# Kernel optimization log

Hardware: AMD Instinct MI355X
Metric: run time of the kernel (lower is better)

Reference implementation:

```python
import jax, jax.numpy as jnp
import numpy as np

B = 64        # number of graphs in the batch
NPG = 1024    # nodes per graph (uniform batch_num_nodes)
N = B * NPG   # total nodes = 65536
D = 512       # input feature dim
DEG = 32      # average degree
K = 0.5       # keep-percent
DROP = NPG - int(np.ceil(K * NPG))  # number of lowest-score nodes zeroed per graph


def setup_inputs() -> dict:
    key = jax.random.key(0)
    k1, k2, k3, k4 = jax.random.split(key, 4)
    features = jax.random.normal(k1, (N, D), dtype=jnp.float32)
    # edges constrained inside each graph's node block (batched DGL graph is block-diagonal)
    offsets = (jnp.arange(B, dtype=jnp.int64) * NPG)[:, None]
    src = (jax.random.randint(k2, (B, NPG * DEG), 0, NPG, dtype=jnp.int64) + offsets).reshape(-1)
    dst = (jax.random.randint(k3, (B, NPG * DEG), 0, NPG, dtype=jnp.int64) + offsets).reshape(-1)
    # GraphConv(input_dim=D, out=1) parameters (glorot-ish scale)
    weight = jax.random.normal(k4, (D, 1), dtype=jnp.float32) * (1.0 / np.sqrt(D))
    bias = jnp.zeros((1,), dtype=jnp.float32)
    return {"features": features, "src": src, "dst": dst, "weight": weight, "bias": bias}


def reference(features, src, dst, weight, bias):
    # --- GraphConv(D -> 1, norm=True, bias=True, activation=relu) ---
    # old-DGL norm=True: symmetric normalization with in-degrees, norm=deg^-0.5 (0 for isolated)
    deg = jnp.zeros((N,), features.dtype).at[dst].add(1.0)
    norm = jnp.where(deg > 0, deg ** -0.5, 0.0)[:, None]          # [N,1]
    # in_feats > out_feats: project first, then aggregate scalars
    h = (features @ weight) * norm                                # [N,1]
    agg = jnp.zeros_like(h).at[dst].add(h[src])                   # sum over in-edges
    w = jax.nn.relu(agg * norm + bias)                            # [N,1] scores
    # --- per-graph top-k masking: zero the DROP smallest scores in each graph ---
    wb = w.reshape(B, NPG)
    ranks = jnp.argsort(jnp.argsort(wb, axis=1), axis=1)          # rank 0 = smallest
    wb = jnp.where(ranks < DROP, jnp.zeros((), wb.dtype), wb)
    # --- elementwise gating of features by (masked) scores ---
    return features * wb.reshape(N, 1)
```

## Files before the change

kernel.cpp:

```cpp
#include <hip/hip_runtime.h>

#define NTOT 65536
#define DIM  512
#define BGR  64
#define NPG  1024
#define DROPN 512
#define SLICES 8
#define MV_BLOCKS 2048

typedef float vf4 __attribute__((ext_vector_type(4)));
typedef unsigned long long u64;

__global__ __launch_bounds__(256) void k1_matvec_deg(
        const float* __restrict__ X, const float* __restrict__ W,
        const int* __restrict__ dst,
        float* __restrict__ p, int* __restrict__ deg_part, int epg) {
    __shared__ int dl[NPG];
    if (blockIdx.x < MV_BLOCKS) {
        const int lane = threadIdx.x & 63;
        const int wid  = (blockIdx.x * 256 + threadIdx.x) >> 6;
        const int nw   = (MV_BLOCKS * 256) >> 6;
        const vf4* wr = (const vf4*)W;
        const vf4 w0 = wr[lane], w1 = wr[lane + 64];
        for (int row = wid; row < NTOT; row += 2 * nw) {
            const int row2 = row + nw;
            const vf4* xr0 = (const vf4*)(X + (size_t)row  * DIM);
            const vf4* xr1 = (const vf4*)(X + (size_t)row2 * DIM);
            vf4 a0 = xr0[lane], a1 = xr0[lane + 64];
            vf4 b0 = xr1[lane], b1 = xr1[lane + 64];
            vf4 m0 = a0 * w0 + a1 * w1;
            vf4 m1 = b0 * w0 + b1 * w1;
            float s0 = m0[0] + m0[1] + m0[2] + m0[3];
            float s1 = m1[0] + m1[1] + m1[2] + m1[3];
            #pragma unroll
            for (int off = 32; off > 0; off >>= 1) {
                s0 += __shfl_down(s0, off, 64);
                s1 += __shfl_down(s1, off, 64);
            }
            if (lane == 0) { p[row] = s0; p[row2] = s1; }
        }
    } else {
        const int b = blockIdx.x - MV_BLOCKS;
        const int g = b & (BGR - 1);
        const int slice = b >> 6;
        const int nbase = g * NPG;
        const int eps = epg / SLICES;
        for (int i = threadIdx.x; i < NPG; i += 256) dl[i] = 0;
        __syncthreads();
        const int4* d4 = (const int4*)(dst + (size_t)g * epg + (size_t)slice * eps);
        const int n4 = eps >> 2;
        for (int i = threadIdx.x; i < n4; i += 256) {
            int4 d = d4[i];
            atomicAdd(&dl[d.x - nbase], 1);
            atomicAdd(&dl[d.y - nbase], 1);
            atomicAdd(&dl[d.z - nbase], 1);
            atomicAdd(&dl[d.w - nbase], 1);
        }
        __syncthreads();
        int* out = deg_part + (size_t)slice * NTOT + nbase;
        for (int i = threadIdx.x; i < NPG; i += 256) out[i] = dl[i];
    }
}

__global__ __launch_bounds__(256) void k2_agg(
        const int* __restrict__ src, const int* __restrict__ dst,
        const float* __restrict__ p, const int* __restrict__ deg_part,
        float* __restrict__ agg_part, float* __restrict__ norm_out, int epg) {
    __shared__ float hl[NPG];
    __shared__ float al[NPG];
    const int b = blockIdx.x;
    const int g = b & (BGR - 1);
    const int slice = b >> 6;
    const int nbase = g * NPG;
    const int eps = epg / SLICES;
    for (int i = threadIdx.x; i < NPG; i += 256) {
        int d = 0;
        #pragma unroll
        for (int s = 0; s < SLICES; s++) d += deg_part[(size_t)s * NTOT + nbase + i];
        float nrm = d > 0 ? (1.0f / sqrtf((float)d)) : 0.f;
        hl[i] = p[nbase + i] * nrm;
        al[i] = 0.f;
        if (slice == 0) norm_out[nbase + i] = nrm;
    }
    __syncthreads();
    const int4* s4 = (const int4*)(src + (size_t)g * epg + (size_t)slice * eps);
    const int4* d4 = (const int4*)(dst + (size_t)g * epg + (size_t)slice * eps);
    const int n4 = eps >> 2;
    for (int i = threadIdx.x; i < n4; i += 256) {
        int4 s = s4[i];
        int4 d = d4[i];
        atomicAdd(&al[d.x - nbase], hl[s.x - nbase]);
        atomicAdd(&al[d.y - nbase], hl[s.y - nbase]);
        atomicAdd(&al[d.z - nbase], hl[s.z - nbase]);
        atomicAdd(&al[d.w - nbase], hl[s.w - nbase]);
    }
    __syncthreads();
    float* out = agg_part + (size_t)slice * NTOT + nbase;
    for (int i = threadIdx.x; i < NPG; i += 256) out[i] = al[i];
}

__global__ __launch_bounds__(1024) void k3_topk(
        const float* __restrict__ agg_part, const float* __restrict__ norm,
        const float* __restrict__ bias, float* __restrict__ gate) {
    __shared__ u64 sk[NPG];
    const int g = blockIdx.x;
    const int t = threadIdx.x;
    const int nbase = g * NPG;
    float a = 0.f;
    #pragma unroll
    for (int s = 0; s < SLICES; s++) a += agg_part[(size_t)s * NTOT + nbase + t];
    float w = a * norm[nbase + t] + bias[0];
    w = w > 0.f ? w : 0.f;
    u64 key = ((u64)__float_as_uint(w) << 32) | (unsigned int)t;

    for (int k = 2; k <= NPG; k <<= 1) {
        const bool up = ((t & k) == 0);
        for (int j = k >> 1; j >= 64; j >>= 1) {
            sk[t] = key;
            __syncthreads();
            u64 partner = sk[t ^ j];
            __syncthreads();
            bool takeMin = (((t & j) == 0) == up);
            key = takeMin ? (key < partner ? key : partner)
                          : (key > partner ? key : partner);
        }
        for (int j = ((k >> 1) < 32 ? (k >> 1) : 32); j >= 1; j >>= 1) {
            u64 partner = (u64)__shfl_xor((long long)key, j, 64);
            bool takeMin = (((t & j) == 0) == up);
            key = takeMin ? (key < partner ? key : partner)
                          : (key > partner ? key : partner);
        }
    }
    int idx = (int)(key & 0xffffffffull);
    float wv = __uint_as_float((unsigned int)(key >> 32));
    gate[nbase + idx] = (t < DROPN) ? 0.f : wv;
}

__global__ __launch_bounds__(256) void k4_gate(
        const float* __restrict__ X, const float* __restrict__ gate,
        float* __restrict__ out) {
    const int lane = threadIdx.x & 63;
    const int nw   = (gridDim.x * blockDim.x) >> 6;
    const int wid  = (blockIdx.x * blockDim.x + threadIdx.x) >> 6;
    for (int row = wid; row < NTOT; row += nw) {
        float g = gate[row];
        vf4* o = (vf4*)(out + (size_t)row * DIM);
        if (g == 0.f) {
            vf4 z = (vf4){0.f, 0.f, 0.f, 0.f};
            o[lane] = z;
            o[lane + 64] = z;
        } else {
            const vf4* xr = (const vf4*)(X + (size_t)row * DIM);
            o[lane]      = xr[lane] * g;
            o[lane + 64] = xr[lane + 64] * g;
        }
    }
}

extern "C" void kernel_launch(void* const* d_in, const int* in_sizes, int n_in,
                              void* d_out, int out_size, void* d_ws, size_t ws_size,
                              hipStream_t stream) {
    const float* X    = (const float*)d_in[0];
    const int*   src  = (const int*)d_in[1];
    const int*   dst  = (const int*)d_in[2];
    const float* W    = (const float*)d_in[3];
    const float* bias = (const float*)d_in[4];
    float* out = (float*)d_out;
    int E   = in_sizes[1];
    int epg = E / BGR;

    float* ws       = (float*)d_ws;
    float* p        = ws;
    float* norm     = ws + 1 * NTOT;
    float* gate     = ws + 2 * NTOT;
    int*   deg_part = (int*)(ws + 3 * NTOT);
    float* agg_part = ws + (3 + SLICES) * NTOT;

    k1_matvec_deg<<<MV_BLOCKS + BGR * SLICES, 256, 0, stream>>>(X, W, dst, p, deg_part, epg);
    k2_agg<<<BGR * SLICES, 256, 0, stream>>>(src, dst, p, deg_part, agg_part, norm, epg);
    k3_topk<<<BGR, 1024, 0, stream>>>(agg_part, norm, bias, gate);
    k4_gate<<<2048, 256, 0, stream>>>(X, gate, out);
}
```

Measured before the change: 280.2 us.

## Fuse all four stages into one cooperative kernel with grid syncs

```diff
diff --git a/kernel.cpp b/kernel.cpp
--- a/kernel.cpp
+++ b/kernel.cpp
@@ -1,29 +1,44 @@
 #include <hip/hip_runtime.h>
+#include <hip/hip_cooperative_groups.h>
+
+namespace cg = cooperative_groups;
 
 #define NTOT 65536
 #define DIM  512
 #define BGR  64
 #define NPG  1024
 #define DROPN 512
-#define SLICES 8
-#define MV_BLOCKS 2048
+#define SLICES 4
+#define NBLK 256
+#define NTHR 1024
 
 typedef float vf4 __attribute__((ext_vector_type(4)));
 typedef unsigned long long u64;
 
-__global__ __launch_bounds__(256) void k1_matvec_deg(
+__global__ __launch_bounds__(NTHR, 4) void fused_all(
         const float* __restrict__ X, const float* __restrict__ W,
-        const int* __restrict__ dst,
-        float* __restrict__ p, int* __restrict__ deg_part, int epg) {
-    __shared__ int dl[NPG];
-    if (blockIdx.x < MV_BLOCKS) {
-        const int lane = threadIdx.x & 63;
-        const int wid  = (blockIdx.x * 256 + threadIdx.x) >> 6;
-        const int nw   = (MV_BLOCKS * 256) >> 6;
+        const int* __restrict__ src, const int* __restrict__ dst,
+        const float* __restrict__ bias,
+        float* __restrict__ p, float* __restrict__ norm,
+        int* __restrict__ deg_part, float* __restrict__ agg_part,
+        float* __restrict__ gate, float* __restrict__ out, int epg) {
+    cg::grid_group grid = cg::this_grid();
+    __shared__ u64 smem64[NPG];
+
+    const int t       = threadIdx.x;
+    const int lane    = t & 63;
+    const int gw      = blockIdx.x * (NTHR / 64) + (t >> 6);
+    const int NW      = NBLK * (NTHR / 64);
+    const int g       = blockIdx.x & (BGR - 1);
+    const int slice   = blockIdx.x >> 6;
+    const int nbase   = g * NPG;
+    const int eps     = epg / SLICES;
+
+    {
         const vf4* wr = (const vf4*)W;
         const vf4 w0 = wr[lane], w1 = wr[lane + 64];
-        for (int row = wid; row < NTOT; row += 2 * nw) {
-            const int row2 = row + nw;
+        for (int row = gw; row < NTOT; row += 2 * NW) {
+            const int row2 = row + NW;
             const vf4* xr0 = (const vf4*)(X + (size_t)row  * DIM);
             const vf4* xr1 = (const vf4*)(X + (size_t)row2 * DIM);
             vf4 a0 = xr0[lane], a1 = xr0[lane + 64];
@@ -39,17 +54,15 @@
             }
             if (lane == 0) { p[row] = s0; p[row2] = s1; }
         }
-    } else {
-        const int b = blockIdx.x - MV_BLOCKS;
-        const int g = b & (BGR - 1);
-        const int slice = b >> 6;
-        const int nbase = g * NPG;
-        const int eps = epg / SLICES;
-        for (int i = threadIdx.x; i < NPG; i += 256) dl[i] = 0;
+    }
+
+    {
+        int* dl = (int*)smem64;
+        for (int i = t; i < NPG; i += NTHR) dl[i] = 0;
         __syncthreads();
         const int4* d4 = (const int4*)(dst + (size_t)g * epg + (size_t)slice * eps);
         const int n4 = eps >> 2;
-        for (int i = threadIdx.x; i < n4; i += 256) {
+        for (int i = t; i < n4; i += NTHR) {
             int4 d = d4[i];
             atomicAdd(&dl[d.x - nbase], 1);
             atomicAdd(&dl[d.y - nbase], 1);
@@ -57,102 +70,85 @@
             atomicAdd(&dl[d.w - nbase], 1);
         }
         __syncthreads();
-        int* out = deg_part + (size_t)slice * NTOT + nbase;
-        for (int i = threadIdx.x; i < NPG; i += 256) out[i] = dl[i];
+        int* op = deg_part + (size_t)slice * NTOT + nbase;
+        for (int i = t; i < NPG; i += NTHR) op[i] = dl[i];
     }
-}
+    grid.sync();
 
-__global__ __launch_bounds__(256) void k2_agg(
-        const int* __restrict__ src, const int* __restrict__ dst,
-        const float* __restrict__ p, const int* __restrict__ deg_part,
-        float* __restrict__ agg_part, float* __restrict__ norm_out, int epg) {
-    __shared__ float hl[NPG];
-    __shared__ float al[NPG];
-    const int b = blockIdx.x;
-    const int g = b & (BGR - 1);
-    const int slice = b >> 6;
-    const int nbase = g * NPG;
-    const int eps = epg / SLICES;
-    for (int i = threadIdx.x; i < NPG; i += 256) {
-        int d = 0;
+    {
+        float* hl = (float*)smem64;
+        float* al = ((float*)smem64) + NPG;
+        for (int i = t; i < NPG; i += NTHR) {
+            int d = 0;
+            #pragma unroll
+            for (int s = 0; s < SLICES; s++) d += deg_part[(size_t)s * NTOT + nbase + i];
+            float nr = d > 0 ? (1.0f / sqrtf((float)d)) : 0.f;
+            hl[i] = p[nbase + i] * nr;
+            al[i] = 0.f;
+            if (slice == 0) norm[nbase + i] = nr;
+        }
+        __syncthreads();
+        const int4* s4 = (const int4*)(src + (size_t)g * epg + (size_t)slice * eps);
+        const int4* d4 = (const int4*)(dst + (size_t)g * epg + (size_t)slice * eps);
+        const int n4 = eps >> 2;
+        for (int i = t; i < n4; i += NTHR) {
+            int4 s = s4[i];
+            int4 d = d4[i];
+            atomicAdd(&al[d.x - nbase], hl[s.x - nbase]);
+            atomicAdd(&al[d.y - nbase], hl[s.y - nbase]);
+            atomicAdd(&al[d.z - nbase], hl[s.z - nbase]);
+            atomicAdd(&al[d.w - nbase], hl[s.w - nbase]);
+        }
+        __syncthreads();
+        float* op = agg_part + (size_t)slice * NTOT + nbase;
+        for (int i = t; i < NPG; i += NTHR) op[i] = al[i];
+    }
+    grid.sync();
+
+    if (blockIdx.x < BGR) {
+        u64* sk = smem64;
+        const int nb2 = blockIdx.x * NPG;
+        float a = 0.f;
         #pragma unroll
-        for (int s = 0; s < SLICES; s++) d += deg_part[(size_t)s * NTOT + nbase + i];
-        float nrm = d > 0 ? (1.0f / sqrtf((float)d)) : 0.f;
-        hl[i] = p[nbase + i] * nrm;
-        al[i] = 0.f;
-        if (slice == 0) norm_out[nbase + i] = nrm;
+        for (int s = 0; s < SLICES; s++) a += agg_part[(size_t)s * NTOT + nb2 + t];
+        float w = a * norm[nb2 + t] + bias[0];
+        w = w > 0.f ? w : 0.f;
+        u64 key = ((u64)__float_as_uint(w) << 32) | (unsigned int)t;
+        for (int k = 2; k <= NPG; k <<= 1) {
+            const bool up = ((t & k) == 0);
+            for (int j = k >> 1; j >= 64; j >>= 1) {
+                sk[t] = key;
+                __syncthreads();
+                u64 partner = sk[t ^ j];
+                __syncthreads();
+                bool takeMin = (((t & j) == 0) == up);
+                key = takeMin ? (key < partner ? key : partner)
+                              : (key > partner ? key : partner);
+            }
+            for (int j = ((k >> 1) < 32 ? (k >> 1) : 32); j >= 1; j >>= 1) {
+                u64 partner = (u64)__shfl_xor((long long)key, j, 64);
+                bool takeMin = (((t & j) == 0) == up);
+                key = takeMin ? (key < partner ? key : partner)
+                              : (key > partner ? key : partner);
+            }
+        }
+        int idx = (int)(key & 0xffffffffull);
+        float wv = __uint_as_float((unsigned int)(key >> 32));
+        gate[nb2 + idx] = (t < DROPN) ? 0.f : wv;
     }
-    __syncthreads();
-    const int4* s4 = (const int4*)(src + (size_t)g * epg + (size_t)slice * eps);
-    const int4* d4 = (const int4*)(dst + (size_t)g * epg + (size_t)slice * eps);
-    const int n4 = eps >> 2;
-    for (int i = threadIdx.x; i < n4; i += 256) {
-        int4 s = s4[i];
-        int4 d = d4[i];
-        atomicAdd(&al[d.x - nbase], hl[s.x - nbase]);
-        atomicAdd(&al[d.y - nbase], hl[s.y - nbase]);
-        atomicAdd(&al[d.z - nbase], hl[s.z - nbase]);
-        atomicAdd(&al[d.w - nbase], hl[s.w - nbase]);
-    }
-    __syncthreads();
-    float* out = agg_part + (size_t)slice * NTOT + nbase;
-    for (int i = threadIdx.x; i < NPG; i += 256) out[i] = al[i];
-}
+    grid.sync();
 
-__global__ __launch_bounds__(1024) void k3_topk(
-        const float* __restrict__ agg_part, const float* __restrict__ norm,
-        const float* __restrict__ bias, float* __restrict__ gate) {
-    __shared__ u64 sk[NPG];
-    const int g = blockIdx.x;
-    const int t = threadIdx.x;
-    const int nbase = g * NPG;
-    float a = 0.f;
-    #pragma unroll
-    for (int s = 0; s < SLICES; s++) a += agg_part[(size_t)s * NTOT + nbase + t];
-    float w = a * norm[nbase + t] + bias[0];
-    w = w > 0.f ? w : 0.f;
-    u64 key = ((u64)__float_as_uint(w) << 32) | (unsigned int)t;
-
-    for (int k = 2; k <= NPG; k <<= 1) {
-        const bool up = ((t & k) == 0);
-        for (int j = k >> 1; j >= 64; j >>= 1) {
-            sk[t] = key;
-            __syncthreads();
-            u64 partner = sk[t ^ j];
-            __syncthreads();
-            bool takeMin = (((t & j) == 0) == up);
-            key = takeMin ? (key < partner ? key : partner)
-                          : (key > partner ? key : partner);
-        }
-        for (int j = ((k >> 1) < 32 ? (k >> 1) : 32); j >= 1; j >>= 1) {
-            u64 partner = (u64)__shfl_xor((long long)key, j, 64);
-            bool takeMin = (((t & j) == 0) == up);
-            key = takeMin ? (key < partner ? key : partner)
-                          : (key > partner ? key : partner);
-        }
-    }
-    int idx = (int)(key & 0xffffffffull);
-    float wv = __uint_as_float((unsigned int)(key >> 32));
-    gate[nbase + idx] = (t < DROPN) ? 0.f : wv;
-}
-
-__global__ __launch_bounds__(256) void k4_gate(
-        const float* __restrict__ X, const float* __restrict__ gate,
-        float* __restrict__ out) {
-    const int lane = threadIdx.x & 63;
-    const int nw   = (gridDim.x * blockDim.x) >> 6;
-    const int wid  = (blockIdx.x * blockDim.x + threadIdx.x) >> 6;
-    for (int row = wid; row < NTOT; row += nw) {
-        float g = gate[row];
+    for (int row = gw; row < NTOT; row += NW) {
+        float gv = gate[row];
         vf4* o = (vf4*)(out + (size_t)row * DIM);
-        if (g == 0.f) {
+        if (gv == 0.f) {
             vf4 z = (vf4){0.f, 0.f, 0.f, 0.f};
             o[lane] = z;
             o[lane + 64] = z;
         } else {
             const vf4* xr = (const vf4*)(X + (size_t)row * DIM);
-            o[lane]      = xr[lane] * g;
-            o[lane + 64] = xr[lane + 64] * g;
+            o[lane]      = xr[lane] * gv;
+            o[lane + 64] = xr[lane + 64] * gv;
         }
     }
 }
@@ -176,8 +172,11 @@
     int*   deg_part = (int*)(ws + 3 * NTOT);
     float* agg_part = ws + (3 + SLICES) * NTOT;
 
-    k1_matvec_deg<<<MV_BLOCKS + BGR * SLICES, 256, 0, stream>>>(X, W, dst, p, deg_part, epg);
-    k2_agg<<<BGR * SLICES, 256, 0, stream>>>(src, dst, p, deg_part, agg_part, norm, epg);
-    k3_topk<<<BGR, 1024, 0, stream>>>(agg_part, norm, bias, gate);
-    k4_gate<<<2048, 256, 0, stream>>>(X, gate, out);
+    void* args[] = {
+        (void*)&X, (void*)&W, (void*)&src, (void*)&dst, (void*)&bias,
+        (void*)&p, (void*)&norm, (void*)&deg_part, (void*)&agg_part,
+        (void*)&gate, (void*)&out, (void*)&epg
+    };
+    hipLaunchCooperativeKernel((void*)fused_all, dim3(NBLK), dim3(NTHR),
+                               args, 0, stream);
 }
```

After: 368.0 us. 1.31x slower.
